# Kernel tuning notes

Measured on AMD Instinct MI355X. Metric: run time of the kernel, lower is better.

The kernel has to match this reference:

```python
import jax, jax.numpy as jnp
import numpy as np

EPS = 1e-6

def _linear_params(key, d_in, d_out):
    w = jax.random.normal(key, (d_in, d_out), dtype=jnp.float32) * np.sqrt(2.0 / (d_in + d_out))
    b = jnp.zeros((d_out,), dtype=jnp.float32)
    return w, b

def setup_inputs() -> dict:
    key = jax.random.key(0)
    ks = jax.random.split(key, 8)
    B, S, D = 4, 2048, 1024
    x = jax.random.normal(ks[0], (B, S, D), dtype=jnp.float32)
    wq, bq = _linear_params(ks[1], D, D)
    wk, bk = _linear_params(ks[2], D, D)
    wv, bv = _linear_params(ks[3], D, D)
    wo, bo = _linear_params(ks[4], D, D)
    w1, b1 = _linear_params(ks[5], D, D)
    w2, b2 = _linear_params(ks[6], D, D)
    g1 = jnp.ones((D,), jnp.float32); be1 = jnp.zeros((D,), jnp.float32)
    g2 = jnp.ones((D,), jnp.float32); be2 = jnp.zeros((D,), jnp.float32)
    return {"x": x, "wq": wq, "bq": bq, "wk": wk, "bk": bk, "wv": wv, "bv": bv,
            "wo": wo, "bo": bo, "w1": w1, "b1": b1, "w2": w2, "b2": b2,
            "g1": g1, "be1": be1, "g2": g2, "be2": be2}

def _layernorm(x, gamma, beta):
    mean = jnp.mean(x, axis=-1, keepdims=True)
    # torch .std() default is unbiased (ddof=1); eps added to std (not var)
    std = jnp.std(x, axis=-1, keepdims=True, ddof=1)
    return gamma * (x - mean) / (std + EPS) + beta

def _attention(x, wq, bq, wk, bk, wv, bv, wo, bo):
    S = x.shape[-2]
    q = x @ wq + bq  # [B,S,D]
    k = x @ wk + bk
    v = x @ wv + bv
    scores = jnp.einsum('bsd,btd->bst', q, k) / jnp.sqrt(jnp.asarray(S, jnp.float32))
    causal = jnp.tril(jnp.ones((S, S), dtype=bool))  # keep lower triangle incl. diag
    scores = jnp.where(causal, scores, -jnp.inf)
    attn = jax.nn.softmax(scores, axis=-1)
    out = jnp.einsum('bst,btd->bsd', attn, v)
    return out @ wo + bo

def reference(x, wq, bq, wk, bk, wv, bv, wo, bo, w1, b1, w2, b2, g1, be1, g2, be2):
    h = _attention(_layernorm(x, g1, be1), wq, bq, wk, bk, wv, bv, wo, bo) + x
    m = _layernorm(h, g2, be2)
    m = jnp.maximum(m @ w1 + b1, 0.0) @ w2 + b2
    return m + h
```

## Files before the change

### kernel.cpp

```cpp
#include <hip/hip_runtime.h>
#include <math.h>

#define BB 4
#define SS 2048
#define DD 1024
#define MM (BB*SS)
#define SD ((size_t)SS*DD)
#define MD ((size_t)MM*DD)
#define PPB ((size_t)2162688)

#define WT_OFF (3*MD + 4*PPB)
#define ZP_OFF (WT_OFF + 6*(size_t)DD*DD)
#define LF_OFF (ZP_OFF + 16)
#define REQ_WS ((LF_OFF + 16384) * 2)

constexpr float LN_EPS = 1e-6f;

typedef __attribute__((ext_vector_type(8))) __bf16 bf16x8;
typedef __attribute__((ext_vector_type(4))) float f32x4;

__device__ __forceinline__ unsigned short f2bfbits(float f){
    unsigned u = __float_as_uint(f);
    u += 0x7FFFu + ((u >> 16) & 1u);
    return (unsigned short)(u >> 16);
}
__device__ __forceinline__ int rowWidth(int s){ return ((s >> 6) + 1) << 6; }
__device__ __forceinline__ size_t rowOff(int s){
    int g = s >> 6;
    return (size_t)4096 * (size_t)((g * (g + 1)) >> 1) + (size_t)(s & 63) * (size_t)((g + 1) << 6);
}
__device__ __forceinline__ void gl_lds(const unsigned short* g, unsigned short* l){
    __builtin_amdgcn_global_load_lds(
        (const __attribute__((address_space(1))) unsigned int*)g,
        (__attribute__((address_space(3))) unsigned int*)l, 16, 0, 0);
}

__device__ __forceinline__ int3 xcd_swz(){
    const int gx = gridDim.x, gy = gridDim.y, gz = gridDim.z;
    const int n = gx * gy * gz;
    int lin = blockIdx.x + gx * (blockIdx.y + gy * blockIdx.z);
    const int cpx = n >> 3;
    lin = (lin & 7) * cpx + (lin >> 3);
    int3 r;
    r.x = lin % gx; lin /= gx;
    r.y = lin % gy;
    r.z = lin / gy;
    return r;
}

__global__ __launch_bounds__(256)
void sentinel_kernel(float* __restrict__ out, const float val){
    out[(size_t)blockIdx.x * 256 + threadIdx.x] = val;
}

struct WPack { const float* w[6]; unsigned short* o[6]; unsigned short* zp; float* lf; };
struct PrepArgs { WPack wp; const float* x; const float* g1; const float* be1;
                  unsigned short* ln; };
__global__ __launch_bounds__(256)
void prep(PrepArgs pa)
{
    const int id = blockIdx.x;
    const int tid = threadIdx.x;
    if (id < 1536){
        __shared__ float Ts[64][65];
        const int z = id >> 8, rem = id & 255;
        const int yy = rem >> 4, xx = rem & 15;
        const float* W = pa.wp.w[z];
        unsigned short* WT = pa.wp.o[z];
        const int r0 = yy*64, c0 = xx*64;
        if (id == 0 && tid < 16) pa.wp.zp[tid] = 0;
        if (id < 16){
            float2 z2 = {0.f, 0.f};
            ((float2*)pa.wp.lf)[id*256 + tid] = z2;
        }
        #pragma unroll
        for (int i = 0; i < 16; ++i){
            int lin = tid + i*256;
            int r = lin >> 6, c = lin & 63;
            Ts[r][c] = W[(size_t)(r0+r)*DD + c0+c];
        }
        __syncthreads();
        #pragma unroll
        for (int i = 0; i < 16; ++i){
            int lin = tid + i*256;
            int r = lin >> 6, c = lin & 63;
            WT[(size_t)(c0+r)*DD + r0+c] = f2bfbits(Ts[c][r]);
        }
    } else {
        __shared__ float red[4];
        const int row = id - 1536;
        float4 xv = ((const float4*)(pa.x + (size_t)row*DD))[tid];
        float v[4] = {xv.x, xv.y, xv.z, xv.w};
        float s = v[0]+v[1]+v[2]+v[3];
        #pragma unroll
        for (int off = 32; off > 0; off >>= 1) s += __shfl_down(s, off, 64);
        if ((tid & 63) == 0) red[tid >> 6] = s;
        __syncthreads();
        const float mean = (red[0]+red[1]+red[2]+red[3]) * (1.0f/DD);
        __syncthreads();
        float q = 0.f;
        #pragma unroll
        for (int i = 0; i < 4; ++i){ float d = v[i]-mean; q += d*d; }
        #pragma unroll
        for (int off = 32; off > 0; off >>= 1) q += __shfl_down(q, off, 64);
        if ((tid & 63) == 0) red[tid >> 6] = q;
        __syncthreads();
        const float var = (red[0]+red[1]+red[2]+red[3]) * (1.0f/(DD-1));
        const float inv = 1.0f/(sqrtf(var) + LN_EPS);
        float4 g4 = ((const float4*)pa.g1)[tid];
        float4 b4 = ((const float4*)pa.be1)[tid];
        ushort4 o;
        o.x = f2bfbits(g4.x*(v[0]-mean)*inv + b4.x);
        o.y = f2bfbits(g4.y*(v[1]-mean)*inv + b4.y);
        o.z = f2bfbits(g4.z*(v[2]-mean)*inv + b4.z);
        o.w = f2bfbits(g4.w*(v[3]-mean)*inv + b4.w);
        ((ushort4*)(pa.ln + (size_t)row*DD))[tid] = o;
    }
}

__global__ __launch_bounds__(256)
void ln_f32(const float* __restrict__ x, const float* __restrict__ gamma,
            const float* __restrict__ beta, unsigned short* __restrict__ out)
{
    __shared__ float red[4];
    const int row = blockIdx.x;
    const int tid = threadIdx.x;
    float4 xv = ((const float4*)(x + (size_t)row*DD))[tid];
    float v[4] = {xv.x, xv.y, xv.z, xv.w};
    float s = v[0]+v[1]+v[2]+v[3];
    #pragma unroll
    for (int off = 32; off > 0; off >>= 1) s += __shfl_down(s, off, 64);
    if ((tid & 63) == 0) red[tid >> 6] = s;
    __syncthreads();
    const float mean = (red[0]+red[1]+red[2]+red[3]) * (1.0f/DD);
    __syncthreads();
    float q = 0.f;
    #pragma unroll
    for (int i = 0; i < 4; ++i){ float d = v[i]-mean; q += d*d; }
    #pragma unroll
    for (int off = 32; off > 0; off >>= 1) q += __shfl_down(q, off, 64);
    if ((tid & 63) == 0) red[tid >> 6] = q;
    __syncthreads();
    const float var = (red[0]+red[1]+red[2]+red[3]) * (1.0f/(DD-1));
    const float inv = 1.0f/(sqrtf(var) + LN_EPS);
    float4 g4 = ((const float4*)gamma)[tid];
    float4 b4 = ((const float4*)beta)[tid];
    ushort4 o;
    o.x = f2bfbits(g4.x*(v[0]-mean)*inv + b4.x);
    o.y = f2bfbits(g4.y*(v[1]-mean)*inv + b4.y);
    o.z = f2bfbits(g4.z*(v[2]-mean)*inv + b4.z);
    o.w = f2bfbits(g4.w*(v[3]-mean)*inv + b4.w);
    ((ushort4*)(out + (size_t)row*DD))[tid] = o;
}

template<bool RELU, bool RES, bool OUTF, bool BIAS_M>
__device__ __forceinline__ void gemm_core(
    const unsigned short* __restrict__ A, const unsigned short* __restrict__ B,
    const float* __restrict__ bias, const float* __restrict__ resF,
    unsigned short* __restrict__ outB, float* __restrict__ outF,
    const int N, const int K, const int lda, const int ldb,
    const int m0, const int n0,
    unsigned short* As, unsigned short* Bs)
{
    const int tid = threadIdx.x, lane = tid & 63, wave = tid >> 6;
    const int wm = ((wave >> 1) & 1) * 64, wn = (wave & 1) * 64;
    const int quad = lane >> 4, l15 = lane & 15;
    const unsigned short* ga[4]; const unsigned short* gb[4];
    #pragma unroll
    for (int c = 0; c < 4; ++c){
        const int mr = (wave*4 + c)*8 + (lane >> 3);
        const int gk = ((lane & 7) - mr) & 7;
        ga[c] = A + (size_t)(m0 + mr)*lda + gk*8;
        gb[c] = B + (size_t)(n0 + mr)*ldb + gk*8;
    }
    f32x4 acc[4][4] = {};
    for (int k0 = 0; k0 < K; k0 += 64){
        #pragma unroll
        for (int c = 0; c < 4; ++c){
            gl_lds(ga[c] + k0, &As[(wave*4+c)*512]);
            gl_lds(gb[c] + k0, &Bs[(wave*4+c)*512]);
        }
        __syncthreads();
        #pragma unroll
        for (int kk = 0; kk < 2; ++kk){
            bf16x8 af[4], bfr[4];
            #pragma unroll
            for (int t = 0; t < 4; ++t){
                const int ra = wm + t*16 + l15, rb = wn + t*16 + l15, gi = kk*4 + quad;
                af[t]  = *(const bf16x8*)&As[ra*64 + (((gi + ra) & 7) << 3)];
                bfr[t] = *(const bf16x8*)&Bs[rb*64 + (((gi + rb) & 7) << 3)];
            }
            #pragma unroll
            for (int i = 0; i < 4; ++i)
                #pragma unroll
                for (int j = 0; j < 4; ++j)
                    acc[i][j] = __builtin_amdgcn_mfma_f32_16x16x32_bf16(af[i], bfr[j], acc[i][j], 0, 0, 0);
        }
        __syncthreads();
    }
    #pragma unroll
    for (int i = 0; i < 4; ++i){
        #pragma unroll
        for (int r = 0; r < 4; ++r){
            const int m = m0 + wm + i*16 + quad*4 + r;
            const float bm = BIAS_M ? bias[m] : 0.f;
            #pragma unroll
            for (int j = 0; j < 4; ++j){
                const int n = n0 + wn + j*16 + l15;
                float v = acc[i][j][r] + (BIAS_M ? bm : bias[n]);
                if constexpr (RELU) v = fmaxf(v, 0.f);
                if constexpr (RES) v += resF[(size_t)m*N + n];
                if constexpr (OUTF) outF[(size_t)m*N + n] = v;
                else outB[(size_t)m*N + n] = f2bfbits(v);
            }
        }
    }
}

template<bool RELU, bool RES, bool OUTF, bool BIAS_M>
__global__ __launch_bounds__(256)
void gemm_mfma(const unsigned short* __restrict__ A, const unsigned short* __restrict__ B,
               const float* __restrict__ bias, const float* __restrict__ resF,
               unsigned short* __restrict__ outB, float* __restrict__ outF,
               const int N, const int K, const int lda, const int ldb)
{
    __shared__ unsigned short As[128*64];
    __shared__ unsigned short Bs[128*64];
    const int3 b = xcd_swz();
    gemm_core<RELU,RES,OUTF,BIAS_M>(A, B, bias, resF, outB, outF, N, K, lda, ldb,
                                    b.y*128, b.x*128, As, Bs);
}

__global__ __launch_bounds__(256)
void proj_fused(const unsigned short* __restrict__ LN,
                const unsigned short* __restrict__ WqT, const unsigned short* __restrict__ WkT,
                const unsigned short* __restrict__ WvT,
                const float* __restrict__ bq, const float* __restrict__ bk,
                const float* __restrict__ bv,
                unsigned short* __restrict__ Qw, unsigned short* __restrict__ Kw,
                unsigned short* __restrict__ VTw)
{
    __shared__ unsigned short As[128*64];
    __shared__ unsigned short Bs[128*64];
    const int lin = blockIdx.x;
    const int id = (lin & 7) * 192 + (lin >> 3);
    if (id < 1024){
        const bool isK = (id >= 512);
        const int q = id & 511;
        const int n0 = (q & 7) * 128, m0 = (q >> 3) * 128;
        gemm_core<false,false,false,false>(LN, isK ? WkT : WqT, isK ? bk : bq, nullptr,
                                           isK ? Kw : Qw, nullptr, DD, DD, DD, DD,
                                           m0, n0, As, Bs);
    } else {
        const int q = id - 1024;
        const int n0 = (q & 63) * 128, m0 = (q >> 6) * 128;
        gemm_core<false,false,false,true>(WvT, LN, bv, nullptr, VTw, nullptr,
                                          MM, DD, DD, DD, m0, n0, As, Bs);
    }
}

__global__ __launch_bounds__(256)
void scores_mfma(const unsigned short* __restrict__ Qb, const unsigned short* __restrict__ Kb,
                 unsigned short* __restrict__ Pb, float* __restrict__ Lf, const float scale)
{
    const int lin = blockIdx.x;
    const int id = (lin & 7) * 68 + (lin >> 3);
    const int z = id / 136;
    const int idx = id - z * 136;
    int y = (int)((sqrtf(8.f * (float)idx + 1.f) - 1.f) * 0.5f);
    while ((y + 1) * (y + 2) / 2 <= idx) ++y;
    while (y * (y + 1) / 2 > idx) --y;
    const int x = idx - y * (y + 1) / 2;
    const int s0 = y * 128, t0 = x * 128;

    const unsigned short* Q  = Qb + (size_t)z*SD;
    const unsigned short* Km = Kb + (size_t)z*SD;
    unsigned short* P        = Pb + (size_t)z*PPB;
    float* L                 = Lf + (size_t)z*SS;
    __shared__ unsigned short As[128*64];
    __shared__ unsigned short Bs[128*64];
    const int tid = threadIdx.x, lane = tid & 63, wave = tid >> 6;
    const int wm = ((wave >> 1) & 1) * 64, wn = (wave & 1) * 64;
    const int quad = lane >> 4, l15 = lane & 15;
    const unsigned short* ga[4]; const unsigned short* gb[4];
    #pragma unroll
    for (int c = 0; c < 4; ++c){
        const int mr = (wave*4 + c)*8 + (lane >> 3);
        const int gk = ((lane & 7) - mr) & 7;
        ga[c] = Q  + (size_t)(s0 + mr)*DD + gk*8;
        gb[c] = Km + (size_t)(t0 + mr)*DD + gk*8;
    }
    f32x4 acc[4][4] = {};
    for (int k0 = 0; k0 < DD; k0 += 64){
        #pragma unroll
        for (int c = 0; c < 4; ++c){
            gl_lds(ga[c] + k0, &As[(wave*4+c)*512]);
            gl_lds(gb[c] + k0, &Bs[(wave*4+c)*512]);
        }
        __syncthreads();
        #pragma unroll
        for (int kk = 0; kk < 2; ++kk){
            bf16x8 af[4], bfr[4];
            #pragma unroll
            for (int t = 0; t < 4; ++t){
                const int ra = wm + t*16 + l15, rb = wn + t*16 + l15, gi = kk*4 + quad;
                af[t]  = *(const bf16x8*)&As[ra*64 + (((gi + ra) & 7) << 3)];
                bfr[t] = *(const bf16x8*)&Bs[rb*64 + (((gi + rb) & 7) << 3)];
            }
            #pragma unroll
            for (int i = 0; i < 4; ++i)
                #pragma unroll
                for (int j = 0; j < 4; ++j)
                    acc[i][j] = __builtin_amdgcn_mfma_f32_16x16x32_bf16(af[i], bfr[j], acc[i][j], 0, 0, 0);
        }
        __syncthreads();
    }
    #pragma unroll
    for (int i = 0; i < 4; ++i){
        #pragma unroll
        for (int r = 0; r < 4; ++r){
            const int s = s0 + wm + i*16 + quad*4 + r;
            const int width = rowWidth(s);
            unsigned short* pr = P + rowOff(s);
            float psum = 0.f;
            if (t0 + wn < width){
                #pragma unroll
                for (int j = 0; j < 4; ++j){
                    const int t = t0 + wn + j*16 + l15;
                    const float e = (t <= s) ? __expf(acc[i][j][r] * scale) : 0.f;
                    pr[t] = f2bfbits(e);
                    psum += e;
                }
                #pragma unroll
                for (int off = 8; off > 0; off >>= 1) psum += __shfl_xor(psum, off, 64);
                if (l15 == 0) atomicAdd(&L[s], psum);
            }
        }
    }
}

__global__ __launch_bounds__(256)
void pv_mfma(const unsigned short* __restrict__ Pb, const unsigned short* __restrict__ VT,
             unsigned short* __restrict__ Cb, const unsigned short* __restrict__ zpad,
             const float* __restrict__ Lf)
{
    const int yr = blockIdx.y;
    const int y  = (blockIdx.z >= 2) ? (15 - yr) : yr;
    const int s0 = y*128, n0 = blockIdx.x*128;
    const unsigned short* P = Pb + (size_t)blockIdx.z*PPB;
    unsigned short* C       = Cb + (size_t)blockIdx.z*SD;
    const float* L          = Lf + (size_t)blockIdx.z*SS;
    const int bcol = blockIdx.z*SS;
    __shared__ unsigned short As[128*64];
    __shared__ unsigned short Bs[128*64];
    const int tid = threadIdx.x, lane = tid & 63, wave = tid >> 6;
    const int wm = ((wave >> 1) & 1) * 64, wn = (wave & 1) * 64;
    const int quad = lane >> 4, l15 = lane & 15;
    const unsigned short* ga[4]; const unsigned short* gb[4]; int pw[4];
    #pragma unroll
    for (int c = 0; c < 4; ++c){
        const int mr = (wave*4 + c)*8 + (lane >> 3);
        const int gk = ((lane & 7) - mr) & 7;
        const int s = s0 + mr;
        pw[c] = rowWidth(s) - gk*8;
        ga[c] = P + rowOff(s) + gk*8;
        gb[c] = VT + (size_t)(n0 + mr)*MM + bcol + gk*8;
    }
    f32x4 acc[4][4] = {};
    const int kmax = s0 + 128;
    for (int k0 = 0; k0 < kmax; k0 += 64){
        #pragma unroll
        for (int c = 0; c < 4; ++c){
            const unsigned short* gp = (k0 < pw[c]) ? (ga[c] + k0) : zpad;
            gl_lds(gp, &As[(wave*4+c)*512]);
            gl_lds(gb[c] + k0, &Bs[(wave*4+c)*512]);
        }
        __syncthreads();
        #pragma unroll
        for (int kk = 0; kk < 2; ++kk){
            bf16x8 af[4], bfr[4];
            #pragma unroll
            for (int t = 0; t < 4; ++t){
                const int ra = wm + t*16 + l15, rb = wn + t*16 + l15, gi = kk*4 + quad;
                af[t]  = *(const bf16x8*)&As[ra*64 + (((gi + ra) & 7) << 3)];
                bfr[t] = *(const bf16x8*)&Bs[rb*64 + (((gi + rb) & 7) << 3)];
            }
            #pragma unroll
            for (int i = 0; i < 4; ++i)
                #pragma unroll
                for (int j = 0; j < 4; ++j)
                    acc[i][j] = __builtin_amdgcn_mfma_f32_16x16x32_bf16(af[i], bfr[j], acc[i][j], 0, 0, 0);
        }
        __syncthreads();
    }
    #pragma unroll
    for (int i = 0; i < 4; ++i){
        #pragma unroll
        for (int r = 0; r < 4; ++r){
            const int s = s0 + wm + i*16 + quad*4 + r;
            const float linv = 1.0f / L[s];
            #pragma unroll
            for (int j = 0; j < 4; ++j){
                const int n = n0 + wn + j*16 + l15;
                C[(size_t)s*DD + n] = f2bfbits(acc[i][j][r] * linv);
            }
        }
    }
}

extern "C" void kernel_launch(void* const* d_in, const int* in_sizes, int n_in,
                              void* d_out, int out_size, void* d_ws, size_t ws_size,
                              hipStream_t stream)
{
    (void)in_sizes; (void)n_in; (void)out_size;
    const float* x   = (const float*)d_in[0];
    const float* bq  = (const float*)d_in[2];
    const float* bk  = (const float*)d_in[4];
    const float* bv  = (const float*)d_in[6];
    const float* bo  = (const float*)d_in[8];
    const float* b1  = (const float*)d_in[10];
    const float* b2  = (const float*)d_in[12];
    const float* g1  = (const float*)d_in[13];
    const float* be1 = (const float*)d_in[14];
    const float* g2  = (const float*)d_in[15];
    const float* be2 = (const float*)d_in[16];
    float* outf = (float*)d_out;

    if (ws_size < (size_t)REQ_WS){
        sentinel_kernel<<<dim3((unsigned)(MD/256)), dim3(256), 0, stream>>>(outf, 1.0e9f);
        return;
    }

    unsigned short* wsb = (unsigned short*)d_ws;
    unsigned short* Qw  = wsb;
    unsigned short* Kw  = wsb + MD;
    unsigned short* VTw = wsb + 2*MD;
    unsigned short* Pw  = wsb + 3*MD;
    unsigned short* WT  = wsb + WT_OFF;
    unsigned short* ZP  = wsb + ZP_OFF;
    float*          Lf  = (float*)(wsb + LF_OFF);
    float*          Hf  = (float*)Kw;
    unsigned short* CTX = Qw;
    unsigned short* MIDw= Pw;
    unsigned short* LN  = (unsigned short*)d_out;

    PrepArgs pa;
    static const int widx[6] = {1,3,5,7,9,11};
    for (int i = 0; i < 6; ++i){
        pa.wp.w[i] = (const float*)d_in[widx[i]];
        pa.wp.o[i] = WT + (size_t)i*DD*DD;
    }
    pa.wp.zp = ZP;
    pa.wp.lf = Lf;
    pa.x = x; pa.g1 = g1; pa.be1 = be1; pa.ln = LN;
    unsigned short* WqT = pa.wp.o[0]; unsigned short* WkT = pa.wp.o[1];
    unsigned short* WvT = pa.wp.o[2]; unsigned short* WoT = pa.wp.o[3];
    unsigned short* W1T = pa.wp.o[4]; unsigned short* W2T = pa.wp.o[5];

    const dim3 blk(256);
    const float scale = 1.0f / sqrtf((float)SS);
    const dim3 gA(DD/128, MM/128);

    prep<<<dim3(1536 + MM), blk, 0, stream>>>(pa);
    proj_fused<<<dim3(1536), blk, 0, stream>>>(LN, WqT, WkT, WvT, bq, bk, bv, Qw, Kw, VTw);
    scores_mfma<<<dim3(544), blk, 0, stream>>>(Qw, Kw, Pw, Lf, scale);
    pv_mfma<<<dim3(DD/128, SS/128, BB), blk, 0, stream>>>(Pw, VTw, CTX, ZP, Lf);
    gemm_mfma<false,true,true,false><<<gA, blk, 0, stream>>>(CTX, WoT, bo, x, nullptr, Hf, DD, DD, DD, DD);
    ln_f32<<<dim3(MM), blk, 0, stream>>>(Hf, g2, be2, LN);
    gemm_mfma<true,false,false,false><<<gA, blk, 0, stream>>>(LN, W1T, b1, nullptr, MIDw, nullptr, DD, DD, DD, DD);
    gemm_mfma<false,true,true,false><<<gA, blk, 0, stream>>>(MIDw, W2T, b2, Hf, nullptr, outf, DD, DD, DD, DD);
}
```

Baseline: 363.4 us.

## Double-buffer LDS tiles in all MFMA GEMM kernels to overlap loads with compute

Replaces the single-buffered load-sync-compute-sync loop in the GEMM, projection, scores and PV kernels with a shared double-buffered pipeline. The next K-tile is prefetched into a second LDS buffer while the current one is consumed, using partial vmcnt waits and raw barriers. The goal is to hide global-to-LDS load latency behind MFMA work. LDS use per block doubles to 64 KB, which can lower occupancy, and the loop assumes an even tile count.

```diff
diff --git a/kernel.cpp b/kernel.cpp
--- a/kernel.cpp
+++ b/kernel.cpp
@@ -153,6 +153,82 @@
     ((ushort4*)(out + (size_t)row*DD))[tid] = o;
 }
 
+template<bool PACKED>
+__device__ __forceinline__ void mfma_db(
+    const unsigned short* const ga[4], const unsigned short* const gb[4],
+    const int* pw, const unsigned short* zpad, const int NT,
+    f32x4 acc[4][4], const int wave, const int lane,
+    unsigned short (&As0)[8192], unsigned short (&Bs0)[8192],
+    unsigned short (&As1)[8192], unsigned short (&Bs1)[8192])
+{
+    const int quad = lane >> 4, l15 = lane & 15;
+    const int wm = ((wave >> 1) & 1) * 64, wn = (wave & 1) * 64;
+
+    auto stage = [&](unsigned short (&Ab)[8192], unsigned short (&Bb)[8192], const int koff){
+        #pragma unroll
+        for (int c = 0; c < 4; ++c){
+            const unsigned short* gp = ga[c] + koff;
+            if constexpr (PACKED) { if (koff >= pw[c]) gp = zpad; }
+            gl_lds(gp, &Ab[(wave*4+c)*512]);
+            gl_lds(gb[c] + koff, &Bb[(wave*4+c)*512]);
+        }
+    };
+    auto compute = [&](unsigned short (&Ab)[8192], unsigned short (&Bb)[8192]){
+        #pragma unroll
+        for (int kk = 0; kk < 2; ++kk){
+            bf16x8 af[4], bfr[4];
+            #pragma unroll
+            for (int t = 0; t < 4; ++t){
+                const int ra = wm + t*16 + l15, rb = wn + t*16 + l15, gi = kk*4 + quad;
+                af[t]  = *(const bf16x8*)&Ab[ra*64 + (((gi + ra) & 7) << 3)];
+                bfr[t] = *(const bf16x8*)&Bb[rb*64 + (((gi + rb) & 7) << 3)];
+            }
+            #pragma unroll
+            for (int i = 0; i < 4; ++i)
+                #pragma unroll
+                for (int j = 0; j < 4; ++j)
+                    acc[i][j] = __builtin_amdgcn_mfma_f32_16x16x32_bf16(af[i], bfr[j], acc[i][j], 0, 0, 0);
+        }
+    };
+
+    stage(As0, Bs0, 0);
+    const int half = NT >> 1;
+    for (int i = 0; i < half; ++i){
+        stage(As1, Bs1, (2*i + 1) << 6);
+        asm volatile("s_waitcnt vmcnt(8)" ::: "memory");
+        __builtin_amdgcn_s_barrier();
+        __builtin_amdgcn_sched_barrier(0);
+        compute(As0, Bs0);
+        __builtin_amdgcn_s_barrier();
+        if (i + 1 < half){
+            stage(As0, Bs0, (2*i + 2) << 6);
+            asm volatile("s_waitcnt vmcnt(8)" ::: "memory");
+        } else {
+            asm volatile("s_waitcnt vmcnt(0)" ::: "memory");
+        }
+        __builtin_amdgcn_s_barrier();
+        __builtin_amdgcn_sched_barrier(0);
+        compute(As1, Bs1);
+        __builtin_amdgcn_s_barrier();
+    }
+}
+
+__device__ __forceinline__ void mk_chunks(const unsigned short* base, size_t ld, int r0,
+                                          int wave, int lane, const unsigned short* g[4]){
+    #pragma unroll
+    for (int c = 0; c < 4; ++c){
+        const int mr = (wave*4 + c)*8 + (lane >> 3);
+        const int gk = ((lane & 7) - mr) & 7;
+        g[c] = base + (size_t)(r0 + mr)*ld + gk*8;
+    }
+}
+
+#define DECL_DB \
+    __shared__ unsigned short As0[8192]; \
+    __shared__ unsigned short Bs0[8192]; \
+    __shared__ unsigned short As1[8192]; \
+    __shared__ unsigned short Bs1[8192];
+
 template<bool RELU, bool RES, bool OUTF, bool BIAS_M>
 __device__ __forceinline__ void gemm_core(
     const unsigned short* __restrict__ A, const unsigned short* __restrict__ B,
@@ -160,44 +236,17 @@
     unsigned short* __restrict__ outB, float* __restrict__ outF,
     const int N, const int K, const int lda, const int ldb,
     const int m0, const int n0,
-    unsigned short* As, unsigned short* Bs)
+    unsigned short (&As0)[8192], unsigned short (&Bs0)[8192],
+    unsigned short (&As1)[8192], unsigned short (&Bs1)[8192])
 {
     const int tid = threadIdx.x, lane = tid & 63, wave = tid >> 6;
     const int wm = ((wave >> 1) & 1) * 64, wn = (wave & 1) * 64;
     const int quad = lane >> 4, l15 = lane & 15;
     const unsigned short* ga[4]; const unsigned short* gb[4];
-    #pragma unroll
-    for (int c = 0; c < 4; ++c){
-        const int mr = (wave*4 + c)*8 + (lane >> 3);
-        const int gk = ((lane & 7) - mr) & 7;
-        ga[c] = A + (size_t)(m0 + mr)*lda + gk*8;
-        gb[c] = B + (size_t)(n0 + mr)*ldb + gk*8;
-    }
+    mk_chunks(A, lda, m0, wave, lane, ga);
+    mk_chunks(B, ldb, n0, wave, lane, gb);
     f32x4 acc[4][4] = {};
-    for (int k0 = 0; k0 < K; k0 += 64){
-        #pragma unroll
-        for (int c = 0; c < 4; ++c){
-            gl_lds(ga[c] + k0, &As[(wave*4+c)*512]);
-            gl_lds(gb[c] + k0, &Bs[(wave*4+c)*512]);
-        }
-        __syncthreads();
-        #pragma unroll
-        for (int kk = 0; kk < 2; ++kk){
-            bf16x8 af[4], bfr[4];
-            #pragma unroll
-            for (int t = 0; t < 4; ++t){
-                const int ra = wm + t*16 + l15, rb = wn + t*16 + l15, gi = kk*4 + quad;
-                af[t]  = *(const bf16x8*)&As[ra*64 + (((gi + ra) & 7) << 3)];
-                bfr[t] = *(const bf16x8*)&Bs[rb*64 + (((gi + rb) & 7) << 3)];
-            }
-            #pragma unroll
-            for (int i = 0; i < 4; ++i)
-                #pragma unroll
-                for (int j = 0; j < 4; ++j)
-                    acc[i][j] = __builtin_amdgcn_mfma_f32_16x16x32_bf16(af[i], bfr[j], acc[i][j], 0, 0, 0);
-        }
-        __syncthreads();
-    }
+    mfma_db<false>(ga, gb, nullptr, nullptr, K >> 6, acc, wave, lane, As0, Bs0, As1, Bs1);
     #pragma unroll
     for (int i = 0; i < 4; ++i){
         #pragma unroll
@@ -224,11 +273,10 @@
                unsigned short* __restrict__ outB, float* __restrict__ outF,
                const int N, const int K, const int lda, const int ldb)
 {
-    __shared__ unsigned short As[128*64];
-    __shared__ unsigned short Bs[128*64];
+    DECL_DB
     const int3 b = xcd_swz();
     gemm_core<RELU,RES,OUTF,BIAS_M>(A, B, bias, resF, outB, outF, N, K, lda, ldb,
-                                    b.y*128, b.x*128, As, Bs);
+                                    b.y*128, b.x*128, As0, Bs0, As1, Bs1);
 }
 
 __global__ __launch_bounds__(256)
@@ -240,8 +288,7 @@
                 unsigned short* __restrict__ Qw, unsigned short* __restrict__ Kw,
                 unsigned short* __restrict__ VTw)
 {
-    __shared__ unsigned short As[128*64];
-    __shared__ unsigned short Bs[128*64];
+    DECL_DB
     const int lin = blockIdx.x;
     const int id = (lin & 7) * 192 + (lin >> 3);
     if (id < 1024){
@@ -250,12 +297,12 @@
         const int n0 = (q & 7) * 128, m0 = (q >> 3) * 128;
         gemm_core<false,false,false,false>(LN, isK ? WkT : WqT, isK ? bk : bq, nullptr,
                                            isK ? Kw : Qw, nullptr, DD, DD, DD, DD,
-                                           m0, n0, As, Bs);
+                                           m0, n0, As0, Bs0, As1, Bs1);
     } else {
         const int q = id - 1024;
         const int n0 = (q & 63) * 128, m0 = (q >> 6) * 128;
         gemm_core<false,false,false,true>(WvT, LN, bv, nullptr, VTw, nullptr,
-                                          MM, DD, DD, DD, m0, n0, As, Bs);
+                                          MM, DD, DD, DD, m0, n0, As0, Bs0, As1, Bs1);
     }
 }
 
@@ -277,44 +324,16 @@
     const unsigned short* Km = Kb + (size_t)z*SD;
     unsigned short* P        = Pb + (size_t)z*PPB;
     float* L                 = Lf + (size_t)z*SS;
-    __shared__ unsigned short As[128*64];
-    __shared__ unsigned short Bs[128*64];
+    DECL_DB
     const int tid = threadIdx.x, lane = tid & 63, wave = tid >> 6;
     const int wm = ((wave >> 1) & 1) * 64, wn = (wave & 1) * 64;
     const int quad = lane >> 4, l15 = lane & 15;
     const unsigned short* ga[4]; const unsigned short* gb[4];
-    #pragma unroll
-    for (int c = 0; c < 4; ++c){
-        const int mr = (wave*4 + c)*8 + (lane >> 3);
-        const int gk = ((lane & 7) - mr) & 7;
-        ga[c] = Q  + (size_t)(s0 + mr)*DD + gk*8;
-        gb[c] = Km + (size_t)(t0 + mr)*DD + gk*8;
-    }
+    mk_chunks(Q,  DD, s0, wave, lane, ga);
+    mk_chunks(Km, DD, t0, wave, lane, gb);
     f32x4 acc[4][4] = {};
-    for (int k0 = 0; k0 < DD; k0 += 64){
-        #pragma unroll
-        for (int c = 0; c < 4; ++c){
-            gl_lds(ga[c] + k0, &As[(wave*4+c)*512]);
-            gl_lds(gb[c] + k0, &Bs[(wave*4+c)*512]);
-        }
-        __syncthreads();
-        #pragma unroll
-        for (int kk = 0; kk < 2; ++kk){
-            bf16x8 af[4], bfr[4];
-            #pragma unroll
-            for (int t = 0; t < 4; ++t){
-                const int ra = wm + t*16 + l15, rb = wn + t*16 + l15, gi = kk*4 + quad;
-                af[t]  = *(const bf16x8*)&As[ra*64 + (((gi + ra) & 7) << 3)];
-                bfr[t] = *(const bf16x8*)&Bs[rb*64 + (((gi + rb) & 7) << 3)];
-            }
-            #pragma unroll
-            for (int i = 0; i < 4; ++i)
-                #pragma unroll
-                for (int j = 0; j < 4; ++j)
-                    acc[i][j] = __builtin_amdgcn_mfma_f32_16x16x32_bf16(af[i], bfr[j], acc[i][j], 0, 0, 0);
-        }
-        __syncthreads();
-    }
+    mfma_db<false>(ga, gb, nullptr, nullptr, DD >> 6, acc, wave, lane, As0, Bs0, As1, Bs1);
+
     #pragma unroll
     for (int i = 0; i < 4; ++i){
         #pragma unroll
@@ -351,8 +370,7 @@
     unsigned short* C       = Cb + (size_t)blockIdx.z*SD;
     const float* L          = Lf + (size_t)blockIdx.z*SS;
     const int bcol = blockIdx.z*SS;
-    __shared__ unsigned short As[128*64];
-    __shared__ unsigned short Bs[128*64];
+    DECL_DB
     const int tid = threadIdx.x, lane = tid & 63, wave = tid >> 6;
     const int wm = ((wave >> 1) & 1) * 64, wn = (wave & 1) * 64;
     const int quad = lane >> 4, l15 = lane & 15;
@@ -364,35 +382,12 @@
         const int s = s0 + mr;
         pw[c] = rowWidth(s) - gk*8;
         ga[c] = P + rowOff(s) + gk*8;
-        gb[c] = VT + (size_t)(n0 + mr)*MM + bcol + gk*8;
-    }
+    }
+    mk_chunks(VT + bcol, MM, n0, wave, lane, gb);
     f32x4 acc[4][4] = {};
-    const int kmax = s0 + 128;
-    for (int k0 = 0; k0 < kmax; k0 += 64){
-        #pragma unroll
-        for (int c = 0; c < 4; ++c){
-            const unsigned short* gp = (k0 < pw[c]) ? (ga[c] + k0) : zpad;
-            gl_lds(gp, &As[(wave*4+c)*512]);
-            gl_lds(gb[c] + k0, &Bs[(wave*4+c)*512]);
-        }
-        __syncthreads();
-        #pragma unroll
-        for (int kk = 0; kk < 2; ++kk){
-            bf16x8 af[4], bfr[4];
-            #pragma unroll
-            for (int t = 0; t < 4; ++t){
-                const int ra = wm + t*16 + l15, rb = wn + t*16 + l15, gi = kk*4 + quad;
-                af[t]  = *(const bf16x8*)&As[ra*64 + (((gi + ra) & 7) << 3)];
-                bfr[t] = *(const bf16x8*)&Bs[rb*64 + (((gi + rb) & 7) << 3)];
-            }
-            #pragma unroll
-            for (int i = 0; i < 4; ++i)
-                #pragma unroll
-                for (int j = 0; j < 4; ++j)
-                    acc[i][j] = __builtin_amdgcn_mfma_f32_16x16x32_bf16(af[i], bfr[j], acc[i][j], 0, 0, 0);
-        }
-        __syncthreads();
-    }
+    const int NT = (s0 >> 6) + 2;
+    mfma_db<true>(ga, gb, pw, zpad, NT, acc, wave, lane, As0, Bs0, As1, Bs1);
+
     #pragma unroll
     for (int i = 0; i < 4; ++i){
         #pragma unroll
```

After: 346.4 us. 4.7% less time.
